# Kernel optimization log

Measured on AMD Instinct MI355X. Metric: run time of the kernel, lower is better.

The kernel has to match this reference:

```python
import jax, jax.numpy as jnp
import numpy as np

WIN = (7, 7)
N_HEADS = 4
DIM = 128


def _relative_pos_index(win):
    h, w = win
    coords = np.stack(np.meshgrid(np.arange(h), np.arange(w), indexing='ij'))  # [2,h,w]
    flat = coords.reshape(2, -1)  # [2, h*w]
    rel = flat[:, :, None] - flat[:, None, :]  # [2, N, N]
    rel = rel.transpose(1, 2, 0)
    rel[:, :, 0] += h - 1
    rel[:, :, 1] += w - 1
    rel[:, :, 0] *= 2 * w - 1
    return rel.sum(-1).astype(np.int64)  # [N, N]


def setup_inputs() -> dict:
    key = jax.random.key(0)
    ks = jax.random.split(key, 6)
    B_, N, C = 4096, WIN[0] * WIN[1], DIM
    nW = 64
    table_len = (2 * WIN[0] - 1) * (2 * WIN[1] - 1)  # 169
    return {
        'x': jax.random.normal(ks[0], (B_, N, C), dtype=jnp.float32),
        'mask': jnp.zeros((nW, N, N), dtype=jnp.float32),
        'qkv_w': jax.random.normal(ks[1], (C, 3 * C), dtype=jnp.float32) * 0.02,
        'qkv_b': jnp.zeros((3 * C,), dtype=jnp.float32),
        'proj_w': jax.random.normal(ks[2], (C, C), dtype=jnp.float32) * 0.02,
        'proj_b': jnp.zeros((C,), dtype=jnp.float32),
        'bias_table': jax.random.normal(ks[3], (table_len, N_HEADS), dtype=jnp.float32) * 0.02,
        'rel_index': jnp.asarray(_relative_pos_index(WIN)),  # [N, N] int64
    }


def reference(x, mask, qkv_w, qkv_b, proj_w, proj_b, bias_table, rel_index):
    B_, N, C = x.shape
    H = N_HEADS
    hd = C // H
    scale = hd ** (-0.5)
    # qkv projection -> [3, B_, H, N, hd]
    qkv = (x @ qkv_w + qkv_b).reshape(B_, N, 3, H, hd).transpose(2, 0, 3, 1, 4)
    q, k, v = qkv[0] * scale, qkv[1], qkv[2]
    attn = jnp.einsum('bhnd,bhmd->bhnm', q, k)  # [B_, H, N, N]
    # gathered relative position bias -> [H, N, N]
    bias = bias_table[rel_index.reshape(-1)].reshape(N, N, H).transpose(2, 0, 1)
    attn = attn + bias[None]
    nW = mask.shape[0]
    attn = attn.reshape(-1, nW, H, N, N) + mask[None, :, None, :, :]
    attn = jax.nn.softmax(attn.reshape(-1, H, N, N), axis=-1)
    out = jnp.einsum('bhnm,bhmd->bhnd', attn, v)  # [B_, H, N, hd]
    out = out.transpose(0, 2, 1, 3).reshape(B_, N, C)
    return out @ proj_w + proj_b
```

## Files before the change

### kernel.cpp

```cpp
#include <hip/hip_runtime.h>
#include <hip/hip_bf16.h>

typedef __bf16 bf16x8 __attribute__((ext_vector_type(8)));
typedef __bf16 bf16x4 __attribute__((ext_vector_type(4)));
typedef float f32x4 __attribute__((ext_vector_type(4)));

#define MFMA16(a, b, c) __builtin_amdgcn_mfma_f32_16x16x32_bf16((a), (b), (c), 0, 0, 0)

constexpr int kB = 4096, kN = 49, kC = 128;
constexpr float kScale = 0.17677669529663687f;
constexpr float kLog2e = 1.4426950408889634f;
constexpr float kQScale = kScale * kLog2e;

constexpr size_t WQ_OFF = 0;
constexpr size_t WP_OFF = 98304;
constexpr size_t BP_OFF = 131072;
constexpr size_t MF_OFF = 196608;

__global__ void prep_kernel(const float* __restrict__ qkv_w,
                            const float* __restrict__ proj_w,
                            const float* __restrict__ bias_table,
                            const int* __restrict__ rel_raw,
                            const float* __restrict__ maskp,
                            __bf16* __restrict__ wq, __bf16* __restrict__ wp,
                            float* __restrict__ biasp, int* __restrict__ mf) {
  const int blk = blockIdx.x, t = threadIdx.x;
  const bool is64 = (rel_raw[1] == 0);
  if (blk < 16) {
    const int kk = t >> 6, lane = t & 63, lm = lane & 15;
    const int k0 = kk * 32 + ((lane >> 4) << 3);
    const int qk = blk >> 3, head = (blk >> 1) & 3, dt = blk & 1;
    const int c = qk * 128 + head * 32 + ((lm >> 2) << 3) + dt * 4 + (lm & 3);
    const float s = (qk == 0) ? kQScale : 1.f;
#pragma unroll
    for (int i = 0; i < 8; ++i)
      wq[((blk * 4 + kk) * 64 + lane) * 8 + i] =
          (__bf16)(qkv_w[(k0 + i) * 384 + c] * s);
  } else if (blk < 24) {
    const int kk = t >> 6, lane = t & 63;
    const int k0 = kk * 32 + ((lane >> 4) << 3);
    const int c  = blk * 16 + (lane & 15);
#pragma unroll
    for (int i = 0; i < 8; ++i)
      wq[((blk * 4 + kk) * 64 + lane) * 8 + i] = (__bf16)qkv_w[(k0 + i) * 384 + c];
  } else if (blk < 32) {
    const int nt = blk - 24;
    const int kk = t >> 6, lane = t & 63;
    const int k0 = kk * 32 + ((lane >> 4) << 3);
    const int c  = nt * 16 + (lane & 15);
#pragma unroll
    for (int i = 0; i < 8; ++i)
      wp[((nt * 4 + kk) * 64 + lane) * 8 + i] = (__bf16)proj_w[(k0 + i) * 128 + c];
  } else if (blk < 96) {
    const int e = (blk - 32) * 256 + t;
    const int h = e >> 12, tok = (e >> 6) & 63, key = e & 63;
    float v;
    if (key >= kN) v = -1e30f;
    else if (tok >= kN) v = 0.f;
    else {
      const int flat = tok * kN + key;
      const int idx = is64 ? rel_raw[2 * flat] : rel_raw[flat];
      v = bias_table[idx * 4 + h] * kLog2e;
    }
    biasp[(h * 64 + tok) * 64 + key] = v;
  } else {
    const int base = (blk - 96) * 19208;
    int any = 0;
    for (int e = base + t; e < base + 19208; e += 256)
      any |= (__float_as_uint(maskp[e]) != 0u) ? 1 : 0;
    const int blkany = __syncthreads_or(any);
    if (t == 0) mf[blk - 96] = blkany;
  }
}

__device__ __forceinline__ uint2 pack4(f32x4 v) {
  bf16x4 h;
  h[0] = (__bf16)v[0]; h[1] = (__bf16)v[1]; h[2] = (__bf16)v[2]; h[3] = (__bf16)v[3];
  return *(uint2*)&h;
}

__device__ __forceinline__ bf16x8 cat2(uint2 a, uint2 b) {
  uint4 u;
  u.x = a.x; u.y = a.y; u.z = b.x; u.w = b.y;
  return *(bf16x8*)&u;
}

__global__ __launch_bounds__(256, 4)
void wattn_fused(const float* __restrict__ x, const float* __restrict__ qkv_b,
                 const float* __restrict__ proj_b,
                 const __bf16* __restrict__ wq, const __bf16* __restrict__ wp,
                 const float* __restrict__ biasp, const float* __restrict__ mask,
                 const int* __restrict__ mf, float* __restrict__ out) {
  constexpr int XS = 136, OBS = 136;
  __shared__ __align__(16) __bf16 xb[64 * XS];
  __bf16* ob = xb;

  const int tid = threadIdx.x;
  const int w = tid >> 6, lane = tid & 63, lg = lane >> 4, lm = lane & 15;
  const int b = blockIdx.x;
  const f32x4 zero4 = {0.f, 0.f, 0.f, 0.f};

  const bool hasMask =
      (mf[0] | mf[1] | mf[2] | mf[3] | mf[4] | mf[5] | mf[6] | mf[7]) != 0;

  {
    const float* xp = x + (size_t)b * (kN * kC);
#pragma unroll
    for (int i = 0; i < 8; ++i) {
      const int it = tid + i * 256;
      const int row = it >> 5, col = (it & 31) << 2;
      const int sr = row < kN ? row : (kN - 1);
      f32x4 v = *(const f32x4*)(xp + sr * kC + col);
      bf16x4 h;
      h[0] = (__bf16)v[0]; h[1] = (__bf16)v[1]; h[2] = (__bf16)v[2]; h[3] = (__bf16)v[3];
      *(bf16x4*)(xb + row * XS + col) = h;
    }
  }
  __syncthreads();

#define LDAF(tt, kk) (*(const bf16x8*)(xb + ((tt) * 16 + lm) * XS + (kk) * 32 + lg * 8))

  bf16x8 qf[4], kf[4], vf[2][2];

  {
    uint2 qh[4][2];
#pragma unroll
    for (int dt = 0; dt < 2; ++dt) {
      const int ct = 2 * w + dt;
      bf16x8 wf[4];
#pragma unroll
      for (int kk = 0; kk < 4; ++kk)
        wf[kk] = *(const bf16x8*)(wq + ((size_t)(ct * 4 + kk) * 64 + lane) * 8);
      f32x4 qb4 = *(const f32x4*)(qkv_b + w * 32 + lg * 8 + dt * 4);
#pragma unroll
      for (int j = 0; j < 4; ++j) qb4[j] *= kQScale;
#pragma unroll
      for (int tt = 0; tt < 4; ++tt) {
        f32x4 acc = zero4;
        __builtin_amdgcn_s_setprio(1);
#pragma unroll
        for (int kk = 0; kk < 4; ++kk) acc = MFMA16(wf[kk], LDAF(tt, kk), acc);
        __builtin_amdgcn_s_setprio(0);
#pragma unroll
        for (int j = 0; j < 4; ++j) acc[j] += qb4[j];
        qh[tt][dt] = pack4(acc);
      }
    }
#pragma unroll
    for (int tt = 0; tt < 4; ++tt) qf[tt] = cat2(qh[tt][0], qh[tt][1]);
  }

  {
    uint2 kh[4][2];
#pragma unroll
    for (int dt = 0; dt < 2; ++dt) {
      const int ct = 8 + 2 * w + dt;
      bf16x8 wf[4];
#pragma unroll
      for (int kk = 0; kk < 4; ++kk)
        wf[kk] = *(const bf16x8*)(wq + ((size_t)(ct * 4 + kk) * 64 + lane) * 8);
      f32x4 kb4 = *(const f32x4*)(qkv_b + 128 + w * 32 + lg * 8 + dt * 4);
#pragma unroll
      for (int tt = 0; tt < 4; ++tt) {
        f32x4 acc = zero4;
        __builtin_amdgcn_s_setprio(1);
#pragma unroll
        for (int kk = 0; kk < 4; ++kk) acc = MFMA16(wf[kk], LDAF(tt, kk), acc);
        __builtin_amdgcn_s_setprio(0);
#pragma unroll
        for (int j = 0; j < 4; ++j) acc[j] += kb4[j];
        kh[tt][dt] = pack4(acc);
      }
    }
#pragma unroll
    for (int kt = 0; kt < 4; ++kt) kf[kt] = cat2(kh[kt][0], kh[kt][1]);
  }

  {
    uint2 vh[4][2];
#pragma unroll
    for (int dt = 0; dt < 2; ++dt) {
      const int ct = 16 + 2 * w + dt;
      bf16x8 wf[4];
#pragma unroll
      for (int kk = 0; kk < 4; ++kk)
        wf[kk] = *(const bf16x8*)(wq + ((size_t)(ct * 4 + kk) * 64 + lane) * 8);
      const float vb = qkv_b[256 + w * 32 + dt * 16 + lm];
#pragma unroll
      for (int mt = 0; mt < 4; ++mt) {
        f32x4 acc = zero4;
        __builtin_amdgcn_s_setprio(1);
#pragma unroll
        for (int kk = 0; kk < 4; ++kk) acc = MFMA16(LDAF(mt, kk), wf[kk], acc);
        __builtin_amdgcn_s_setprio(0);
#pragma unroll
        for (int j = 0; j < 4; ++j) acc[j] += vb;
        vh[mt][dt] = pack4(acc);
      }
    }
#pragma unroll
    for (int ks = 0; ks < 2; ++ks)
#pragma unroll
      for (int dt = 0; dt < 2; ++dt)
        vf[ks][dt] = cat2(vh[ks * 2][dt], vh[ks * 2 + 1][dt]);
  }
  __syncthreads();

  const float* bpp = biasp + w * 4096;
  const float* mkp = mask + (size_t)(b & 63) * (kN * kN);

#pragma unroll
  for (int tt = 0; tt < 4; ++tt) {
    f32x4 st[4];
    __builtin_amdgcn_s_setprio(1);
#pragma unroll
    for (int kt = 0; kt < 4; ++kt) st[kt] = MFMA16(kf[kt], qf[tt], zero4);
    __builtin_amdgcn_s_setprio(0);
    const int tok = tt * 16 + lm;
#pragma unroll
    for (int kt = 0; kt < 4; ++kt) {
      f32x4 bm = *(const f32x4*)(bpp + (tok << 6) + kt * 16 + lg * 4);
#pragma unroll
      for (int j = 0; j < 4; ++j) st[kt][j] += bm[j];
    }
    if (hasMask) {
      const int tok2 = tok < kN ? tok : (kN - 1);
#pragma unroll
      for (int kt = 0; kt < 4; ++kt)
#pragma unroll
        for (int j = 0; j < 4; ++j) {
          const int key = kt * 16 + lg * 4 + j;
          const int key2 = key < kN ? key : (kN - 1);
          st[kt][j] += mkp[tok2 * kN + key2] * kLog2e;
        }
    }
    float m = -3e38f;
#pragma unroll
    for (int kt = 0; kt < 4; ++kt)
#pragma unroll
      for (int j = 0; j < 4; ++j) m = fmaxf(m, st[kt][j]);
    m = fmaxf(m, __shfl_xor(m, 16));
    m = fmaxf(m, __shfl_xor(m, 32));
    float sum = 0.f;
#pragma unroll
    for (int kt = 0; kt < 4; ++kt)
#pragma unroll
      for (int j = 0; j < 4; ++j) {
        const float e = exp2f(st[kt][j] - m);
        st[kt][j] = e;
        sum += e;
      }
    sum += __shfl_xor(sum, 16);
    sum += __shfl_xor(sum, 32);
    const float rs = __builtin_amdgcn_rcpf(sum);
    uint2 pst[4];
#pragma unroll
    for (int kt = 0; kt < 4; ++kt) {
      f32x4 t;
#pragma unroll
      for (int j = 0; j < 4; ++j) t[j] = st[kt][j] * rs;
      pst[kt] = pack4(t);
    }
    bf16x8 pa0 = cat2(pst[0], pst[1]);
    bf16x8 pa1 = cat2(pst[2], pst[3]);
#pragma unroll
    for (int dt = 0; dt < 2; ++dt) {
      f32x4 o = MFMA16(pa0, vf[0][dt], zero4);
      o = MFMA16(pa1, vf[1][dt], o);
#pragma unroll
      for (int j = 0; j < 4; ++j)
        ob[(tt * 16 + lg * 4 + j) * OBS + w * 32 + dt * 16 + lm] = (__bf16)o[j];
    }
  }

  bf16x8 wpb[2][4];
#pragma unroll
  for (int n = 0; n < 2; ++n)
#pragma unroll
    for (int kk = 0; kk < 4; ++kk)
      wpb[n][kk] = *(const bf16x8*)(wp + (size_t)(((w * 2 + n) * 4 + kk) * 64 + lane) * 8);

  __syncthreads();

  {
    float* op = out + (size_t)b * (kN * kC);
    const float pb0 = proj_b[(w * 2 + 0) * 16 + lm];
    const float pb1 = proj_b[(w * 2 + 1) * 16 + lm];
#pragma unroll
    for (int mt = 0; mt < 4; ++mt) {
      bf16x8 paf[4];
#pragma unroll
      for (int kk = 0; kk < 4; ++kk)
        paf[kk] = *(const bf16x8*)(ob + (mt * 16 + lm) * OBS + kk * 32 + lg * 8);
      f32x4 a0 = zero4, a1 = zero4;
      __builtin_amdgcn_s_setprio(1);
#pragma unroll
      for (int kk = 0; kk < 4; ++kk) {
        a0 = MFMA16(paf[kk], wpb[0][kk], a0);
        a1 = MFMA16(paf[kk], wpb[1][kk], a1);
      }
      __builtin_amdgcn_s_setprio(0);
#pragma unroll
      for (int j = 0; j < 4; ++j) {
        const int r = mt * 16 + lg * 4 + j;
        if (r < kN) {
          op[r * kC + (w * 2 + 0) * 16 + lm] = a0[j] + pb0;
          op[r * kC + (w * 2 + 1) * 16 + lm] = a1[j] + pb1;
        }
      }
    }
  }
#undef LDAF
}

extern "C" void kernel_launch(void* const* d_in, const int* in_sizes, int n_in,
                              void* d_out, int out_size, void* d_ws, size_t ws_size,
                              hipStream_t stream) {
  const float* x          = (const float*)d_in[0];
  const float* mask       = (const float*)d_in[1];
  const float* qkv_w      = (const float*)d_in[2];
  const float* qkv_b      = (const float*)d_in[3];
  const float* proj_w     = (const float*)d_in[4];
  const float* proj_b     = (const float*)d_in[5];
  const float* bias_table = (const float*)d_in[6];
  const int*   rel        = (const int*)d_in[7];

  char* ws = (char*)d_ws;
  __bf16* wq   = (__bf16*)(ws + WQ_OFF);
  __bf16* wp   = (__bf16*)(ws + WP_OFF);
  float* biasp = (float*)(ws + BP_OFF);
  int*   mf    = (int*)(ws + MF_OFF);

  prep_kernel<<<104, 256, 0, stream>>>(qkv_w, proj_w, bias_table, rel, mask,
                                       wq, wp, biasp, mf);
  wattn_fused<<<kB, 256, 0, stream>>>(x, qkv_b, proj_b, wq, wp, biasp, mask,
                                      mf, (float*)d_out);
}
```

Baseline: 103.8 us.

## Process two windows per block with double-buffered LDS and interleaved stages

Each block now handles two consecutive windows, staging both inputs into separate LDS buffers up front and interleaving the second window's QKV/attention with the first window's output projection. This is meant to hide global load latency and amortise per-block setup such as weight fragment loads and mask flag checks. It halves the grid and doubles LDS per block, which may reduce occupancy or load balance.

New measurement: 124.8 us. 1.2x slower.

```diff
diff --git a/kernel.cpp b/kernel.cpp
--- a/kernel.cpp
+++ b/kernel.cpp
@@ -85,232 +85,264 @@
   return *(bf16x8*)&u;
 }
 
+constexpr int XS = 136, OBS = 136;
+
+struct Frags {
+  bf16x8 qf[4], kf[4], vf[2][2];
+};
+
+__device__ __forceinline__ void stage_x(const float* __restrict__ x, int b,
+                                        __bf16* xbuf, int tid) {
+  const float* xp = x + (size_t)b * (kN * kC);
+#pragma unroll
+  for (int i = 0; i < 8; ++i) {
+    const int it = tid + i * 256;
+    const int row = it >> 5, col = (it & 31) << 2;
+    const int sr = row < kN ? row : (kN - 1);
+    f32x4 v = *(const f32x4*)(xp + sr * kC + col);
+    bf16x4 h;
+    h[0] = (__bf16)v[0]; h[1] = (__bf16)v[1]; h[2] = (__bf16)v[2]; h[3] = (__bf16)v[3];
+    *(bf16x4*)(xbuf + row * XS + col) = h;
+  }
+}
+
+__device__ __forceinline__ void do_qkv(const __bf16* xbuf,
+                                       const __bf16* __restrict__ wq,
+                                       const float* __restrict__ qkv_b,
+                                       int w, int lane, int lg, int lm,
+                                       Frags& F) {
+  const f32x4 zero4 = {0.f, 0.f, 0.f, 0.f};
+#define LDAF(tt, kk) (*(const bf16x8*)(xbuf + ((tt) * 16 + lm) * XS + (kk) * 32 + lg * 8))
+  {
+    uint2 qh[4][2];
+#pragma unroll
+    for (int dt = 0; dt < 2; ++dt) {
+      const int ct = 2 * w + dt;
+      bf16x8 wf[4];
+#pragma unroll
+      for (int kk = 0; kk < 4; ++kk)
+        wf[kk] = *(const bf16x8*)(wq + ((size_t)(ct * 4 + kk) * 64 + lane) * 8);
+      f32x4 qb4 = *(const f32x4*)(qkv_b + w * 32 + lg * 8 + dt * 4);
+#pragma unroll
+      for (int j = 0; j < 4; ++j) qb4[j] *= kQScale;
+#pragma unroll
+      for (int tt = 0; tt < 4; ++tt) {
+        f32x4 acc = zero4;
+        __builtin_amdgcn_s_setprio(1);
+#pragma unroll
+        for (int kk = 0; kk < 4; ++kk) acc = MFMA16(wf[kk], LDAF(tt, kk), acc);
+        __builtin_amdgcn_s_setprio(0);
+#pragma unroll
+        for (int j = 0; j < 4; ++j) acc[j] += qb4[j];
+        qh[tt][dt] = pack4(acc);
+      }
+    }
+#pragma unroll
+    for (int tt = 0; tt < 4; ++tt) F.qf[tt] = cat2(qh[tt][0], qh[tt][1]);
+  }
+  {
+    uint2 kh[4][2];
+#pragma unroll
+    for (int dt = 0; dt < 2; ++dt) {
+      const int ct = 8 + 2 * w + dt;
+      bf16x8 wf[4];
+#pragma unroll
+      for (int kk = 0; kk < 4; ++kk)
+        wf[kk] = *(const bf16x8*)(wq + ((size_t)(ct * 4 + kk) * 64 + lane) * 8);
+      f32x4 kb4 = *(const f32x4*)(qkv_b + 128 + w * 32 + lg * 8 + dt * 4);
+#pragma unroll
+      for (int tt = 0; tt < 4; ++tt) {
+        f32x4 acc = zero4;
+        __builtin_amdgcn_s_setprio(1);
+#pragma unroll
+        for (int kk = 0; kk < 4; ++kk) acc = MFMA16(wf[kk], LDAF(tt, kk), acc);
+        __builtin_amdgcn_s_setprio(0);
+#pragma unroll
+        for (int j = 0; j < 4; ++j) acc[j] += kb4[j];
+        kh[tt][dt] = pack4(acc);
+      }
+    }
+#pragma unroll
+    for (int kt = 0; kt < 4; ++kt) F.kf[kt] = cat2(kh[kt][0], kh[kt][1]);
+  }
+  {
+    uint2 vh[4][2];
+#pragma unroll
+    for (int dt = 0; dt < 2; ++dt) {
+      const int ct = 16 + 2 * w + dt;
+      bf16x8 wf[4];
+#pragma unroll
+      for (int kk = 0; kk < 4; ++kk)
+        wf[kk] = *(const bf16x8*)(wq + ((size_t)(ct * 4 + kk) * 64 + lane) * 8);
+      const float vb = qkv_b[256 + w * 32 + dt * 16 + lm];
+#pragma unroll
+      for (int mt = 0; mt < 4; ++mt) {
+        f32x4 acc = zero4;
+        __builtin_amdgcn_s_setprio(1);
+#pragma unroll
+        for (int kk = 0; kk < 4; ++kk) acc = MFMA16(LDAF(mt, kk), wf[kk], acc);
+        __builtin_amdgcn_s_setprio(0);
+#pragma unroll
+        for (int j = 0; j < 4; ++j) acc[j] += vb;
+        vh[mt][dt] = pack4(acc);
+      }
+    }
+#pragma unroll
+    for (int ks = 0; ks < 2; ++ks)
+#pragma unroll
+      for (int dt = 0; dt < 2; ++dt)
+        F.vf[ks][dt] = cat2(vh[ks * 2][dt], vh[ks * 2 + 1][dt]);
+  }
+#undef LDAF
+}
+
+__device__ __forceinline__ void do_attn(const Frags& F, __bf16* obuf,
+                                        const float* __restrict__ bpp,
+                                        const float* __restrict__ mkp,
+                                        bool hasMask, int w, int lg, int lm) {
+  const f32x4 zero4 = {0.f, 0.f, 0.f, 0.f};
+#pragma unroll
+  for (int tt = 0; tt < 4; ++tt) {
+    f32x4 st[4];
+    __builtin_amdgcn_s_setprio(1);
+#pragma unroll
+    for (int kt = 0; kt < 4; ++kt) st[kt] = MFMA16(F.kf[kt], F.qf[tt], zero4);
+    __builtin_amdgcn_s_setprio(0);
+    const int tok = tt * 16 + lm;
+#pragma unroll
+    for (int kt = 0; kt < 4; ++kt) {
+      f32x4 bm = *(const f32x4*)(bpp + (tok << 6) + kt * 16 + lg * 4);
+#pragma unroll
+      for (int j = 0; j < 4; ++j) st[kt][j] += bm[j];
+    }
+    if (hasMask) {
+      const int tok2 = tok < kN ? tok : (kN - 1);
+#pragma unroll
+      for (int kt = 0; kt < 4; ++kt)
+#pragma unroll
+        for (int j = 0; j < 4; ++j) {
+          const int key = kt * 16 + lg * 4 + j;
+          const int key2 = key < kN ? key : (kN - 1);
+          st[kt][j] += mkp[tok2 * kN + key2] * kLog2e;
+        }
+    }
+    float m = -3e38f;
+#pragma unroll
+    for (int kt = 0; kt < 4; ++kt)
+#pragma unroll
+      for (int j = 0; j < 4; ++j) m = fmaxf(m, st[kt][j]);
+    m = fmaxf(m, __shfl_xor(m, 16));
+    m = fmaxf(m, __shfl_xor(m, 32));
+    float sum = 0.f;
+#pragma unroll
+    for (int kt = 0; kt < 4; ++kt)
+#pragma unroll
+      for (int j = 0; j < 4; ++j) {
+        const float e = exp2f(st[kt][j] - m);
+        st[kt][j] = e;
+        sum += e;
+      }
+    sum += __shfl_xor(sum, 16);
+    sum += __shfl_xor(sum, 32);
+    const float rs = __builtin_amdgcn_rcpf(sum);
+    uint2 pst[4];
+#pragma unroll
+    for (int kt = 0; kt < 4; ++kt) {
+      f32x4 t;
+#pragma unroll
+      for (int j = 0; j < 4; ++j) t[j] = st[kt][j] * rs;
+      pst[kt] = pack4(t);
+    }
+    bf16x8 pa0 = cat2(pst[0], pst[1]);
+    bf16x8 pa1 = cat2(pst[2], pst[3]);
+#pragma unroll
+    for (int dt = 0; dt < 2; ++dt) {
+      f32x4 o = MFMA16(pa0, F.vf[0][dt], zero4);
+      o = MFMA16(pa1, F.vf[1][dt], o);
+#pragma unroll
+      for (int j = 0; j < 4; ++j)
+        obuf[(tt * 16 + lg * 4 + j) * OBS + w * 32 + dt * 16 + lm] = (__bf16)o[j];
+    }
+  }
+}
+
+__device__ __forceinline__ void do_proj(const __bf16* obuf,
+                                        const __bf16* __restrict__ wp,
+                                        const float* __restrict__ proj_b,
+                                        float* __restrict__ op,
+                                        int w, int lane, int lg, int lm) {
+  const f32x4 zero4 = {0.f, 0.f, 0.f, 0.f};
+  bf16x8 wpb[2][4];
+#pragma unroll
+  for (int n = 0; n < 2; ++n)
+#pragma unroll
+    for (int kk = 0; kk < 4; ++kk)
+      wpb[n][kk] = *(const bf16x8*)(wp + (size_t)(((w * 2 + n) * 4 + kk) * 64 + lane) * 8);
+  const float pb0 = proj_b[(w * 2 + 0) * 16 + lm];
+  const float pb1 = proj_b[(w * 2 + 1) * 16 + lm];
+#pragma unroll
+  for (int mt = 0; mt < 4; ++mt) {
+    bf16x8 paf[4];
+#pragma unroll
+    for (int kk = 0; kk < 4; ++kk)
+      paf[kk] = *(const bf16x8*)(obuf + (mt * 16 + lm) * OBS + kk * 32 + lg * 8);
+    f32x4 a0 = zero4, a1 = zero4;
+    __builtin_amdgcn_s_setprio(1);
+#pragma unroll
+    for (int kk = 0; kk < 4; ++kk) {
+      a0 = MFMA16(paf[kk], wpb[0][kk], a0);
+      a1 = MFMA16(paf[kk], wpb[1][kk], a1);
+    }
+    __builtin_amdgcn_s_setprio(0);
+#pragma unroll
+    for (int j = 0; j < 4; ++j) {
+      const int r = mt * 16 + lg * 4 + j;
+      if (r < kN) {
+        op[r * kC + (w * 2 + 0) * 16 + lm] = a0[j] + pb0;
+        op[r * kC + (w * 2 + 1) * 16 + lm] = a1[j] + pb1;
+      }
+    }
+  }
+}
+
 __global__ __launch_bounds__(256, 4)
 void wattn_fused(const float* __restrict__ x, const float* __restrict__ qkv_b,
                  const float* __restrict__ proj_b,
                  const __bf16* __restrict__ wq, const __bf16* __restrict__ wp,
                  const float* __restrict__ biasp, const float* __restrict__ mask,
                  const int* __restrict__ mf, float* __restrict__ out) {
-  constexpr int XS = 136, OBS = 136;
-  __shared__ __align__(16) __bf16 xb[64 * XS];
-  __bf16* ob = xb;
+  __shared__ __align__(16) __bf16 xb[2][64 * XS];
 
   const int tid = threadIdx.x;
   const int w = tid >> 6, lane = tid & 63, lg = lane >> 4, lm = lane & 15;
-  const int b = blockIdx.x;
-  const f32x4 zero4 = {0.f, 0.f, 0.f, 0.f};
+  const int b0 = blockIdx.x * 2, b1 = b0 + 1;
 
   const bool hasMask =
       (mf[0] | mf[1] | mf[2] | mf[3] | mf[4] | mf[5] | mf[6] | mf[7]) != 0;
 
-  {
-    const float* xp = x + (size_t)b * (kN * kC);
-#pragma unroll
-    for (int i = 0; i < 8; ++i) {
-      const int it = tid + i * 256;
-      const int row = it >> 5, col = (it & 31) << 2;
-      const int sr = row < kN ? row : (kN - 1);
-      f32x4 v = *(const f32x4*)(xp + sr * kC + col);
-      bf16x4 h;
-      h[0] = (__bf16)v[0]; h[1] = (__bf16)v[1]; h[2] = (__bf16)v[2]; h[3] = (__bf16)v[3];
-      *(bf16x4*)(xb + row * XS + col) = h;
-    }
-  }
+  const float* bpp = biasp + w * 4096;
+  const float* mk0 = mask + (size_t)(b0 & 63) * (kN * kN);
+  const float* mk1 = mask + (size_t)(b1 & 63) * (kN * kN);
+
+  stage_x(x, b0, xb[0], tid);
+  stage_x(x, b1, xb[1], tid);
   __syncthreads();
 
-#define LDAF(tt, kk) (*(const bf16x8*)(xb + ((tt) * 16 + lm) * XS + (kk) * 32 + lg * 8))
-
-  bf16x8 qf[4], kf[4], vf[2][2];
-
-  {
-    uint2 qh[4][2];
-#pragma unroll
-    for (int dt = 0; dt < 2; ++dt) {
-      const int ct = 2 * w + dt;
-      bf16x8 wf[4];
-#pragma unroll
-      for (int kk = 0; kk < 4; ++kk)
-        wf[kk] = *(const bf16x8*)(wq + ((size_t)(ct * 4 + kk) * 64 + lane) * 8);
-      f32x4 qb4 = *(const f32x4*)(qkv_b + w * 32 + lg * 8 + dt * 4);
-#pragma unroll
-      for (int j = 0; j < 4; ++j) qb4[j] *= kQScale;
-#pragma unroll
-      for (int tt = 0; tt < 4; ++tt) {
-        f32x4 acc = zero4;
-        __builtin_amdgcn_s_setprio(1);
-#pragma unroll
-        for (int kk = 0; kk < 4; ++kk) acc = MFMA16(wf[kk], LDAF(tt, kk), acc);
-        __builtin_amdgcn_s_setprio(0);
-#pragma unroll
-        for (int j = 0; j < 4; ++j) acc[j] += qb4[j];
-        qh[tt][dt] = pack4(acc);
-      }
-    }
-#pragma unroll
-    for (int tt = 0; tt < 4; ++tt) qf[tt] = cat2(qh[tt][0], qh[tt][1]);
-  }
-
-  {
-    uint2 kh[4][2];
-#pragma unroll
-    for (int dt = 0; dt < 2; ++dt) {
-      const int ct = 8 + 2 * w + dt;
-      bf16x8 wf[4];
-#pragma unroll
-      for (int kk = 0; kk < 4; ++kk)
-        wf[kk] = *(const bf16x8*)(wq + ((size_t)(ct * 4 + kk) * 64 + lane) * 8);
-      f32x4 kb4 = *(const f32x4*)(qkv_b + 128 + w * 32 + lg * 8 + dt * 4);
-#pragma unroll
-      for (int tt = 0; tt < 4; ++tt) {
-        f32x4 acc = zero4;
-        __builtin_amdgcn_s_setprio(1);
-#pragma unroll
-        for (int kk = 0; kk < 4; ++kk) acc = MFMA16(wf[kk], LDAF(tt, kk), acc);
-        __builtin_amdgcn_s_setprio(0);
-#pragma unroll
-        for (int j = 0; j < 4; ++j) acc[j] += kb4[j];
-        kh[tt][dt] = pack4(acc);
-      }
-    }
-#pragma unroll
-    for (int kt = 0; kt < 4; ++kt) kf[kt] = cat2(kh[kt][0], kh[kt][1]);
-  }
-
-  {
-    uint2 vh[4][2];
-#pragma unroll
-    for (int dt = 0; dt < 2; ++dt) {
-      const int ct = 16 + 2 * w + dt;
-      bf16x8 wf[4];
-#pragma unroll
-      for (int kk = 0; kk < 4; ++kk)
-        wf[kk] = *(const bf16x8*)(wq + ((size_t)(ct * 4 + kk) * 64 + lane) * 8);
-      const float vb = qkv_b[256 + w * 32 + dt * 16 + lm];
-#pragma unroll
-      for (int mt = 0; mt < 4; ++mt) {
-        f32x4 acc = zero4;
-        __builtin_amdgcn_s_setprio(1);
-#pragma unroll
-        for (int kk = 0; kk < 4; ++kk) acc = MFMA16(LDAF(mt, kk), wf[kk], acc);
-        __builtin_amdgcn_s_setprio(0);
-#pragma unroll
-        for (int j = 0; j < 4; ++j) acc[j] += vb;
-        vh[mt][dt] = pack4(acc);
-      }
-    }
-#pragma unroll
-    for (int ks = 0; ks < 2; ++ks)
-#pragma unroll
-      for (int dt = 0; dt < 2; ++dt)
-        vf[ks][dt] = cat2(vh[ks * 2][dt], vh[ks * 2 + 1][dt]);
+  {
+    Frags F0;
+    do_qkv(xb[0], wq, qkv_b, w, lane, lg, lm, F0);
+    __syncthreads();
+    do_attn(F0, xb[0], bpp, mk0, hasMask, w, lg, lm);
+  }
+  {
+    Frags F1;
+    do_qkv(xb[1], wq, qkv_b, w, lane, lg, lm, F1);
+    __syncthreads();
+    do_attn(F1, xb[1], bpp, mk1, hasMask, w, lg, lm);
+    do_proj(xb[0], wp, proj_b, out + (size_t)b0 * (kN * kC), w, lane, lg, lm);
   }
   __syncthreads();
-
-  const float* bpp = biasp + w * 4096;
-  const float* mkp = mask + (size_t)(b & 63) * (kN * kN);
-
-#pragma unroll
-  for (int tt = 0; tt < 4; ++tt) {
-    f32x4 st[4];
-    __builtin_amdgcn_s_setprio(1);
-#pragma unroll
-    for (int kt = 0; kt < 4; ++kt) st[kt] = MFMA16(kf[kt], qf[tt], zero4);
-    __builtin_amdgcn_s_setprio(0);
-    const int tok = tt * 16 + lm;
-#pragma unroll
-    for (int kt = 0; kt < 4; ++kt) {
-      f32x4 bm = *(const f32x4*)(bpp + (tok << 6) + kt * 16 + lg * 4);
-#pragma unroll
-      for (int j = 0; j < 4; ++j) st[kt][j] += bm[j];
-    }
-    if (hasMask) {
-      const int tok2 = tok < kN ? tok : (kN - 1);
-#pragma unroll
-      for (int kt = 0; kt < 4; ++kt)
-#pragma unroll
-        for (int j = 0; j < 4; ++j) {
-          const int key = kt * 16 + lg * 4 + j;
-          const int key2 = key < kN ? key : (kN - 1);
-          st[kt][j] += mkp[tok2 * kN + key2] * kLog2e;
-        }
-    }
-    float m = -3e38f;
-#pragma unroll
-    for (int kt = 0; kt < 4; ++kt)
-#pragma unroll
-      for (int j = 0; j < 4; ++j) m = fmaxf(m, st[kt][j]);
-    m = fmaxf(m, __shfl_xor(m, 16));
-    m = fmaxf(m, __shfl_xor(m, 32));
-    float sum = 0.f;
-#pragma unroll
-    for (int kt = 0; kt < 4; ++kt)
-#pragma unroll
-      for (int j = 0; j < 4; ++j) {
-        const float e = exp2f(st[kt][j] - m);
-        st[kt][j] = e;
-        sum += e;
-      }
-    sum += __shfl_xor(sum, 16);
-    sum += __shfl_xor(sum, 32);
-    const float rs = __builtin_amdgcn_rcpf(sum);
-    uint2 pst[4];
-#pragma unroll
-    for (int kt = 0; kt < 4; ++kt) {
-      f32x4 t;
-#pragma unroll
-      for (int j = 0; j < 4; ++j) t[j] = st[kt][j] * rs;
-      pst[kt] = pack4(t);
-    }
-    bf16x8 pa0 = cat2(pst[0], pst[1]);
-    bf16x8 pa1 = cat2(pst[2], pst[3]);
-#pragma unroll
-    for (int dt = 0; dt < 2; ++dt) {
-      f32x4 o = MFMA16(pa0, vf[0][dt], zero4);
-      o = MFMA16(pa1, vf[1][dt], o);
-#pragma unroll
-      for (int j = 0; j < 4; ++j)
-        ob[(tt * 16 + lg * 4 + j) * OBS + w * 32 + dt * 16 + lm] = (__bf16)o[j];
-    }
-  }
-
-  bf16x8 wpb[2][4];
-#pragma unroll
-  for (int n = 0; n < 2; ++n)
-#pragma unroll
-    for (int kk = 0; kk < 4; ++kk)
-      wpb[n][kk] = *(const bf16x8*)(wp + (size_t)(((w * 2 + n) * 4 + kk) * 64 + lane) * 8);
-
-  __syncthreads();
-
-  {
-    float* op = out + (size_t)b * (kN * kC);
-    const float pb0 = proj_b[(w * 2 + 0) * 16 + lm];
-    const float pb1 = proj_b[(w * 2 + 1) * 16 + lm];
-#pragma unroll
-    for (int mt = 0; mt < 4; ++mt) {
-      bf16x8 paf[4];
-#pragma unroll
-      for (int kk = 0; kk < 4; ++kk)
-        paf[kk] = *(const bf16x8*)(ob + (mt * 16 + lm) * OBS + kk * 32 + lg * 8);
-      f32x4 a0 = zero4, a1 = zero4;
-      __builtin_amdgcn_s_setprio(1);
-#pragma unroll
-      for (int kk = 0; kk < 4; ++kk) {
-        a0 = MFMA16(paf[kk], wpb[0][kk], a0);
-        a1 = MFMA16(paf[kk], wpb[1][kk], a1);
-      }
-      __builtin_amdgcn_s_setprio(0);
-#pragma unroll
-      for (int j = 0; j < 4; ++j) {
-        const int r = mt * 16 + lg * 4 + j;
-        if (r < kN) {
-          op[r * kC + (w * 2 + 0) * 16 + lm] = a0[j] + pb0;
-          op[r * kC + (w * 2 + 1) * 16 + lm] = a1[j] + pb1;
-        }
-      }
-    }
-  }
-#undef LDAF
+  do_proj(xb[1], wp, proj_b, out + (size_t)b1 * (kN * kC), w, lane, lg, lm);
 }
 
 extern "C" void kernel_launch(void* const* d_in, const int* in_sizes, int n_in,
@@ -333,6 +365,6 @@
 
   prep_kernel<<<104, 256, 0, stream>>>(qkv_w, proj_w, bias_table, rel, mask,
                                        wq, wp, biasp, mf);
-  wattn_fused<<<kB, 256, 0, stream>>>(x, qkv_b, proj_b, wq, wp, biasp, mask,
-                                      mf, (float*)d_out);
-}
+  wattn_fused<<<kB / 2, 256, 0, stream>>>(x, qkv_b, proj_b, wq, wp, biasp,
+                                          mask, mf, (float*)d_out);
+}
```
